# Optimization experiments

Measured on AMD Instinct MI355X. Metric: run time of the kernel, lower is better.

Reference implementation:

```python
import jax, jax.numpy as jnp
import numpy as np

N_NODES = 50000
N_EDGES = 600000
H_DIM = 128
N_RELS = 8
N_BASES = 4


def setup_inputs() -> dict:
    key = jax.random.key(0)
    ks = jax.random.split(key, 12)
    feats = jax.random.normal(ks[0], (N_NODES, H_DIM), dtype=jnp.float32)
    src = jax.random.randint(ks[1], (N_EDGES,), 0, N_NODES, dtype=jnp.int64)
    dst = jax.random.randint(ks[2], (N_EDGES,), 0, N_NODES, dtype=jnp.int64)
    etype = jax.random.randint(ks[3], (N_EDGES,), 0, N_RELS, dtype=jnp.int64)
    norm = jax.random.uniform(ks[4], (N_EDGES, 1), dtype=jnp.float32)
    s = 1.0 / np.sqrt(H_DIM)
    # layer 0 params (basis decomposition: W_r = sum_b comp[r,b] * basis[b])
    basis0 = jax.random.normal(ks[5], (N_BASES, H_DIM, H_DIM), dtype=jnp.float32) * s
    comp0 = jax.random.normal(ks[6], (N_RELS, N_BASES), dtype=jnp.float32)
    bias0 = jnp.zeros((H_DIM,), dtype=jnp.float32)
    # layer 1 params
    basis1 = jax.random.normal(ks[7], (N_BASES, H_DIM, H_DIM), dtype=jnp.float32) * s
    comp1 = jax.random.normal(ks[8], (N_RELS, N_BASES), dtype=jnp.float32)
    bias1 = jnp.zeros((H_DIM,), dtype=jnp.float32)
    return {"feats": feats, "src": src, "dst": dst, "etype": etype, "norm": norm,
            "basis0": basis0, "comp0": comp0, "bias0": bias0,
            "basis1": basis1, "comp1": comp1, "bias1": bias1}


def _rel_graph_conv(h, src, dst, etype, norm, basis, comp, bias):
    # basis-decomposed relation weights: [R, d_in, d_out]
    W = jnp.einsum('rb,bdo->rdo', comp, basis)
    # transform all nodes under every relation: [R, N, d_out]
    Hr = jnp.einsum('nd,rdo->rno', h, W)
    # gather per-edge message by (relation, source node), apply edge norm
    msg = Hr[etype, src] * norm  # [E, d_out]
    # scatter-sum into destination nodes
    agg = jax.ops.segment_sum(msg, dst, num_segments=h.shape[0])
    return jax.nn.relu(agg + bias)


def reference(feats, src, dst, etype, norm, basis0, comp0, bias0, basis1, comp1, bias1):
    h = _rel_graph_conv(feats, src, dst, etype, norm, basis0, comp0, bias0)
    h = _rel_graph_conv(h, src, dst, etype, norm, basis1, comp1, bias1)
    return h
```

## Files before the change

### kernel.cpp

```cpp
#include <hip/hip_runtime.h>

#define H    128
#define NB   4
#define DT   32

typedef __attribute__((ext_vector_type(8))) short short8;
typedef __attribute__((ext_vector_type(4))) float f32x4;

static __device__ __forceinline__ unsigned short f2bf(float f) {
    unsigned u = __float_as_uint(f);
    unsigned r = (u + 0x7fffu + ((u >> 16) & 1u)) >> 16;
    return (unsigned short)r;
}
static __device__ __forceinline__ float bf_lo(unsigned v) {
    return __uint_as_float((v & 0xffffu) << 16);
}
static __device__ __forceinline__ float bf_hi(unsigned v) {
    return __uint_as_float(v & 0xffff0000u);
}
static __device__ __forceinline__ float bfe(short s) {
    return __uint_as_float(((unsigned)(unsigned short)s) << 16);
}

__global__ __launch_bounds__(256) void zero_i(int* __restrict__ p, int n) {
    int i = blockIdx.x * 256 + threadIdx.x;
    if (i < n) p[i] = 0;
}

__global__ __launch_bounds__(256) void hist_rank(const int* __restrict__ dst,
                                                 int* __restrict__ counts,
                                                 int* __restrict__ rank, int E) {
    int e = blockIdx.x * 256 + threadIdx.x;
    if (e < E) rank[e] = atomicAdd(&counts[dst[e]], 1);
}

__global__ __launch_bounds__(1024) void scan_blocks(const int* __restrict__ counts,
                                                    int* __restrict__ partial,
                                                    int* __restrict__ blocksums, int n) {
    __shared__ int buf[1024];
    int tid = threadIdx.x;
    int i = blockIdx.x * 1024 + tid;
    buf[tid] = (i < n) ? counts[i] : 0;
    __syncthreads();
#pragma unroll
    for (int off = 1; off < 1024; off <<= 1) {
        int t = (tid >= off) ? buf[tid - off] : 0;
        __syncthreads();
        buf[tid] += t;
        __syncthreads();
    }
    if (i < n) partial[i] = buf[tid];
    if (tid == 1023) blocksums[blockIdx.x] = buf[1023];
}

__global__ __launch_bounds__(64) void scan_carry(int* __restrict__ blocksums, int nb) {
    int tid = threadIdx.x;
    int v = (tid < nb) ? blocksums[tid] : 0;
#pragma unroll
    for (int off = 1; off < 64; off <<= 1) {
        int t = __shfl_up(v, off);
        if (tid >= off) v += t;
    }
    if (tid < nb) blocksums[tid] = v;
}

__global__ __launch_bounds__(256) void scan_add(const int* __restrict__ partial,
                                                const int* __restrict__ blocksums,
                                                int* __restrict__ offs, int n) {
    int i = blockIdx.x * 256 + threadIdx.x;
    if (i >= n) return;
    int b = i >> 10;
    int carry = (b > 0) ? blocksums[b - 1] : 0;
    offs[i + 1] = partial[i] + carry;
    if (i == 0) offs[0] = 0;
}

__global__ __launch_bounds__(256) void scatter_edges(
        const int* __restrict__ src, const int* __restrict__ dst,
        const int* __restrict__ etype, const float* __restrict__ norm,
        const float* __restrict__ comp0, const float* __restrict__ comp1,
        const int* __restrict__ offs, const int* __restrict__ rank,
        uint4* __restrict__ er0, uint4* __restrict__ er1, int E) {
    int e = blockIdx.x * 256 + threadIdx.x;
    if (e >= E) return;
    int pos = offs[dst[e]] + rank[e];
    float w = norm[e];
    int et = etype[e];
    float4 c0 = *(const float4*)(comp0 + et * NB);
    float4 c1 = *(const float4*)(comp1 + et * NB);
    uint4 r0, r1;
    r0.x = (unsigned)src[e];
    r0.y = (unsigned)f2bf(w * c0.x) | ((unsigned)f2bf(w * c0.y) << 16);
    r0.z = (unsigned)f2bf(w * c0.z) | ((unsigned)f2bf(w * c0.w) << 16);
    r0.w = 0;
    r1.x = (unsigned)src[e];
    r1.y = (unsigned)f2bf(w * c1.x) | ((unsigned)f2bf(w * c1.y) << 16);
    r1.z = (unsigned)f2bf(w * c1.z) | ((unsigned)f2bf(w * c1.w) << 16);
    r1.w = 0;
    er0[pos] = r0;
    er1[pos] = r1;
}

__global__ __launch_bounds__(256) void convert_bf16(const float* __restrict__ in,
                                                    unsigned short* __restrict__ out, int n4) {
    int i = blockIdx.x * 256 + threadIdx.x;
    if (i >= n4) return;
    float4 v = ((const float4*)in)[i];
    ushort4 o;
    o.x = f2bf(v.x); o.y = f2bf(v.y); o.z = f2bf(v.z); o.w = f2bf(v.w);
    ((ushort4*)out)[i] = o;
}

__global__ __launch_bounds__(128) void make_wb(
        const float* __restrict__ basis0, const float* __restrict__ basis1,
        unsigned short* __restrict__ Wb) {
    int b = blockIdx.x;
    int d = blockIdx.y;
    int l = blockIdx.z;
    int o = threadIdx.x;
    const float* basis = l ? basis1 : basis0;
    float s = basis[((size_t)b * H + d) * H + o];
    Wb[((size_t)l * H + o) * (NB * H) + b * H + d] = f2bf(s);
}

#define EDGE_ACC(REC, HV) {                                             \
    float wa = bf_lo(REC.y), wb = bf_hi(REC.y);                         \
    float wc = bf_lo(REC.z), wd = bf_hi(REC.z);                         \
    _Pragma("unroll")                                                   \
    for (int c = 0; c < 8; ++c) {                                       \
        float f = bfe(HV[c]);                                           \
        a0[c] = fmaf(wa, f, a0[c]); a1[c] = fmaf(wb, f, a1[c]);         \
        a2[c] = fmaf(wc, f, a2[c]); a3[c] = fmaf(wd, f, a3[c]);         \
    } }

__global__ __launch_bounds__(512) void fused_layer(
        const unsigned short* __restrict__ hin,
        const int* __restrict__ offs,
        const uint4* __restrict__ er,
        const unsigned short* __restrict__ Wb,
        const float* __restrict__ bias,
        void* __restrict__ outp, int M, int write_bf16) {
    __shared__ char lds[DT * 1024];
    const int tid  = threadIdx.x;
    const int nl   = tid >> 4;
    const int ch   = tid & 15;
    const int v0   = blockIdx.x * DT;
    const int v    = v0 + nl;

    float a0[8], a1[8], a2[8], a3[8];
#pragma unroll
    for (int c = 0; c < 8; ++c) { a0[c] = 0.f; a1[c] = 0.f; a2[c] = 0.f; a3[c] = 0.f; }

    if (v < M) {
        const int beg = offs[v], end = offs[v + 1];
        int e = beg;
        for (; e + 2 <= end; e += 2) {
            uint4 r0 = er[e];
            uint4 r1 = er[e + 1];
            short8 h0 = *(const short8*)(hin + (size_t)r0.x * H + ch * 8);
            short8 h1 = *(const short8*)(hin + (size_t)r1.x * H + ch * 8);
            EDGE_ACC(r0, h0)
            EDGE_ACC(r1, h1)
        }
        if (e < end) {
            uint4 r0 = er[e];
            short8 h0 = *(const short8*)(hin + (size_t)r0.x * H + ch * 8);
            EDGE_ACC(r0, h0)
        }
    }

    {
        char* row = lds + nl * 1024;
        const int swz = (nl & 7) << 4;
        uint4 pk;
#define PACK(A) pk.x = (unsigned)f2bf(A[0]) | ((unsigned)f2bf(A[1]) << 16); \
                pk.y = (unsigned)f2bf(A[2]) | ((unsigned)f2bf(A[3]) << 16); \
                pk.z = (unsigned)f2bf(A[4]) | ((unsigned)f2bf(A[5]) << 16); \
                pk.w = (unsigned)f2bf(A[6]) | ((unsigned)f2bf(A[7]) << 16);
        PACK(a0) *(uint4*)(row + ((0 * 256 + ch * 16) ^ swz)) = pk;
        PACK(a1) *(uint4*)(row + ((1 * 256 + ch * 16) ^ swz)) = pk;
        PACK(a2) *(uint4*)(row + ((2 * 256 + ch * 16) ^ swz)) = pk;
        PACK(a3) *(uint4*)(row + ((3 * 256 + ch * 16) ^ swz)) = pk;
#undef PACK
    }
    __syncthreads();

    const int wid  = tid >> 6;
    const int lane = tid & 63;
    const int n0 = wid * 16;
    const int lr = lane & 15;
    const int lg = lane >> 4;
    const char* bbase = (const char*)Wb + (size_t)(n0 + lr) * (NB * H) * 2;
    const int swz = (lr & 7) << 4;

    f32x4 acc0 = (f32x4){0.f, 0.f, 0.f, 0.f};
    f32x4 acc1 = (f32x4){0.f, 0.f, 0.f, 0.f};
#pragma unroll
    for (int ks = 0; ks < 16; ++ks) {
        const int kb = ks * 64 + lg * 16;
        short8 b  = *(const short8*)(bbase + kb);
        short8 av0 = *(const short8*)(lds + (lr)      * 1024 + (kb ^ swz));
        short8 av1 = *(const short8*)(lds + (16 + lr) * 1024 + (kb ^ swz));
        acc0 = __builtin_amdgcn_mfma_f32_16x16x32_bf16(av0, b, acc0, 0, 0, 0);
        acc1 = __builtin_amdgcn_mfma_f32_16x16x32_bf16(av1, b, acc1, 0, 0, 0);
    }

    const float bcol = bias[n0 + lr];
#pragma unroll
    for (int m = 0; m < 2; ++m) {
        const f32x4 a = m ? acc1 : acc0;
#pragma unroll
        for (int j = 0; j < 4; ++j) {
            const int rl   = m * 16 + lg * 4 + j;
            const int grow = v0 + rl;
            if (grow < M) {
                float val = fmaxf(a[j] + bcol, 0.f);
                if (write_bf16)
                    ((unsigned short*)outp)[(size_t)grow * H + n0 + lr] = f2bf(val);
                else
                    ((float*)outp)[(size_t)grow * H + n0 + lr] = val;
            }
        }
    }
}

extern "C" void kernel_launch(void* const* d_in, const int* in_sizes, int n_in,
                              void* d_out, int out_size, void* d_ws, size_t ws_size,
                              hipStream_t stream) {
    const float* feats  = (const float*)d_in[0];
    const int*   src    = (const int*)  d_in[1];
    const int*   dst    = (const int*)  d_in[2];
    const int*   etype  = (const int*)  d_in[3];
    const float* norm   = (const float*)d_in[4];
    const float* basis0 = (const float*)d_in[5];
    const float* comp0  = (const float*)d_in[6];
    const float* bias0  = (const float*)d_in[7];
    const float* basis1 = (const float*)d_in[8];
    const float* comp1  = (const float*)d_in[9];
    const float* bias1  = (const float*)d_in[10];
    float* out = (float*)d_out;

    const int M = in_sizes[0] / H;
    const int E = in_sizes[1];

    char* ws = (char*)d_ws;
    size_t cur = 0;
    auto take = [&](size_t bytes) { void* p = ws + cur; cur += (bytes + 255) & ~(size_t)255; return p; };
    unsigned short* hbf  = (unsigned short*)take((size_t)M * H * 2);
    unsigned short* h1bf = (unsigned short*)take((size_t)M * H * 2);
    unsigned short* Wb   = (unsigned short*)take((size_t)2 * H * NB * H * 2);
    int*   counts  = (int*)take((size_t)M * 4);
    int*   offs    = (int*)take((size_t)(M + 1) * 4);
    int*   partial = (int*)take((size_t)M * 4);
    int*   bsums   = (int*)take((size_t)64 * 4);
    int*   rank    = (int*)take((size_t)E * 4);
    uint4* er0     = (uint4*)take((size_t)E * 16);
    uint4* er1     = (uint4*)take((size_t)E * 16);

    dim3 blk(256);
    int mb  = (M + 255) / 256;
    int eb  = (E + 255) / 256;
    int n4  = M * H / 4;
    int cb  = (n4 + 255) / 256;
    int nsb = (M + 1023) / 1024;
    int fb  = (M + DT - 1) / DT;

    zero_i       <<<mb, blk, 0, stream>>>(counts, M);
    hist_rank    <<<eb, blk, 0, stream>>>(dst, counts, rank, E);
    scan_blocks  <<<nsb, 1024, 0, stream>>>(counts, partial, bsums, M);
    scan_carry   <<<1, 64, 0, stream>>>(bsums, nsb);
    scan_add     <<<mb, blk, 0, stream>>>(partial, bsums, offs, M);
    scatter_edges<<<eb, blk, 0, stream>>>(src, dst, etype, norm, comp0, comp1,
                                          offs, rank, er0, er1, E);
    convert_bf16 <<<cb, blk, 0, stream>>>(feats, hbf, n4);
    make_wb      <<<dim3(NB, H, 2), 128, 0, stream>>>(basis0, basis1, Wb);

    fused_layer<<<fb, 512, 0, stream>>>(hbf, offs, er0, Wb, bias0, h1bf, M, 1);
    fused_layer<<<fb, 512, 0, stream>>>(h1bf, offs, er1,
                                        Wb + (size_t)H * NB * H, bias1, out, M, 0);
}
```

Baseline: 191.6 us.

## Split each node's edge list across two thread groups and halve node tile

Each block now handles 16 nodes instead of 32, with two 16-thread groups per node taking alternating edges. The two partial bf16 sums are added in LDS before a single 16-row MFMA pass. This doubles the grid size and shortens each thread's serial gather chain, aiming to hide gather latency and balance degree skew better. The cost is half the MFMA work per block plus an extra LDS reduction and barrier, and an additional bf16 rounding of the partial sums. The zeroing kernel is also replaced with hipMemsetAsync.

```diff
diff --git a/kernel.cpp b/kernel.cpp
--- a/kernel.cpp
+++ b/kernel.cpp
@@ -2,7 +2,7 @@
 
 #define H    128
 #define NB   4
-#define DT   32
+#define DT   16
 
 typedef __attribute__((ext_vector_type(8))) short short8;
 typedef __attribute__((ext_vector_type(4))) float f32x4;
@@ -21,10 +21,10 @@
 static __device__ __forceinline__ float bfe(short s) {
     return __uint_as_float(((unsigned)(unsigned short)s) << 16);
 }
-
-__global__ __launch_bounds__(256) void zero_i(int* __restrict__ p, int n) {
-    int i = blockIdx.x * 256 + threadIdx.x;
-    if (i < n) p[i] = 0;
+static __device__ __forceinline__ unsigned bfadd2(unsigned a, unsigned b) {
+    float lo = bf_lo(a) + bf_lo(b);
+    float hi = bf_hi(a) + bf_hi(b);
+    return (unsigned)f2bf(lo) | ((unsigned)f2bf(hi) << 16);
 }
 
 __global__ __launch_bounds__(256) void hist_rank(const int* __restrict__ dst,
@@ -123,7 +123,7 @@
     Wb[((size_t)l * H + o) * (NB * H) + b * H + d] = f2bf(s);
 }
 
-#define EDGE_ACC(REC, HV) {                                             \
+#define EACC(REC, HV) {                                                 \
     float wa = bf_lo(REC.y), wb = bf_hi(REC.y);                         \
     float wc = bf_lo(REC.z), wd = bf_hi(REC.z);                         \
     _Pragma("unroll")                                                   \
@@ -140,12 +140,14 @@
         const unsigned short* __restrict__ Wb,
         const float* __restrict__ bias,
         void* __restrict__ outp, int M, int write_bf16) {
-    __shared__ char lds[DT * 1024];
+    __shared__ char lds[32 * 1024];
     const int tid  = threadIdx.x;
-    const int nl   = tid >> 4;
+    const int slot = tid >> 4;
     const int ch   = tid & 15;
+    const int n    = slot & 15;
+    const int hh   = slot >> 4;
     const int v0   = blockIdx.x * DT;
-    const int v    = v0 + nl;
+    const int v    = v0 + n;
 
     float a0[8], a1[8], a2[8], a3[8];
 #pragma unroll
@@ -153,25 +155,25 @@
 
     if (v < M) {
         const int beg = offs[v], end = offs[v + 1];
-        int e = beg;
-        for (; e + 2 <= end; e += 2) {
+        int e = beg + hh;
+        for (; e + 2 < end; e += 4) {
             uint4 r0 = er[e];
-            uint4 r1 = er[e + 1];
+            uint4 r1 = er[e + 2];
             short8 h0 = *(const short8*)(hin + (size_t)r0.x * H + ch * 8);
             short8 h1 = *(const short8*)(hin + (size_t)r1.x * H + ch * 8);
-            EDGE_ACC(r0, h0)
-            EDGE_ACC(r1, h1)
+            EACC(r0, h0)
+            EACC(r1, h1)
         }
         if (e < end) {
             uint4 r0 = er[e];
             short8 h0 = *(const short8*)(hin + (size_t)r0.x * H + ch * 8);
-            EDGE_ACC(r0, h0)
+            EACC(r0, h0)
         }
     }
 
     {
-        char* row = lds + nl * 1024;
-        const int swz = (nl & 7) << 4;
+        char* row = lds + slot * 1024;
+        const int swz = (slot & 7) << 4;
         uint4 pk;
 #define PACK(A) pk.x = (unsigned)f2bf(A[0]) | ((unsigned)f2bf(A[1]) << 16); \
                 pk.y = (unsigned)f2bf(A[2]) | ((unsigned)f2bf(A[3]) << 16); \
@@ -185,41 +187,52 @@
     }
     __syncthreads();
 
+    {
+        const int mn = tid >> 5;
+        const int mc = tid & 31;
+        char*       p0 = lds + mn * 1024 + mc * 32;
+        const char* p1 = lds + (16 + mn) * 1024 + mc * 32;
+        uint4 x0 = *(uint4*)p0;
+        uint4 x1 = *(const uint4*)p1;
+        uint4 y0 = *(uint4*)(p0 + 16);
+        uint4 y1 = *(const uint4*)(p1 + 16);
+        x0.x = bfadd2(x0.x, x1.x); x0.y = bfadd2(x0.y, x1.y);
+        x0.z = bfadd2(x0.z, x1.z); x0.w = bfadd2(x0.w, x1.w);
+        y0.x = bfadd2(y0.x, y1.x); y0.y = bfadd2(y0.y, y1.y);
+        y0.z = bfadd2(y0.z, y1.z); y0.w = bfadd2(y0.w, y1.w);
+        *(uint4*)p0 = x0;
+        *(uint4*)(p0 + 16) = y0;
+    }
+    __syncthreads();
+
     const int wid  = tid >> 6;
     const int lane = tid & 63;
-    const int n0 = wid * 16;
     const int lr = lane & 15;
     const int lg = lane >> 4;
+    const int n0 = wid * 16;
     const char* bbase = (const char*)Wb + (size_t)(n0 + lr) * (NB * H) * 2;
+    const char* abase = lds + lr * 1024;
     const int swz = (lr & 7) << 4;
 
-    f32x4 acc0 = (f32x4){0.f, 0.f, 0.f, 0.f};
-    f32x4 acc1 = (f32x4){0.f, 0.f, 0.f, 0.f};
+    f32x4 acc = (f32x4){0.f, 0.f, 0.f, 0.f};
 #pragma unroll
     for (int ks = 0; ks < 16; ++ks) {
         const int kb = ks * 64 + lg * 16;
-        short8 b  = *(const short8*)(bbase + kb);
-        short8 av0 = *(const short8*)(lds + (lr)      * 1024 + (kb ^ swz));
-        short8 av1 = *(const short8*)(lds + (16 + lr) * 1024 + (kb ^ swz));
-        acc0 = __builtin_amdgcn_mfma_f32_16x16x32_bf16(av0, b, acc0, 0, 0, 0);
-        acc1 = __builtin_amdgcn_mfma_f32_16x16x32_bf16(av1, b, acc1, 0, 0, 0);
-    }
-
-    const float bcol = bias[n0 + lr];
-#pragma unroll
-    for (int m = 0; m < 2; ++m) {
-        const f32x4 a = m ? acc1 : acc0;
-#pragma unroll
-        for (int j = 0; j < 4; ++j) {
-            const int rl   = m * 16 + lg * 4 + j;
-            const int grow = v0 + rl;
-            if (grow < M) {
-                float val = fmaxf(a[j] + bcol, 0.f);
-                if (write_bf16)
-                    ((unsigned short*)outp)[(size_t)grow * H + n0 + lr] = f2bf(val);
-                else
-                    ((float*)outp)[(size_t)grow * H + n0 + lr] = val;
-            }
+        short8 a = *(const short8*)(abase + (kb ^ swz));
+        short8 b = *(const short8*)(bbase + kb);
+        acc = __builtin_amdgcn_mfma_f32_16x16x32_bf16(a, b, acc, 0, 0, 0);
+    }
+
+    const float bc = bias[n0 + lr];
+#pragma unroll
+    for (int j = 0; j < 4; ++j) {
+        const int grow = v0 + lg * 4 + j;
+        if (grow < M) {
+            float val = fmaxf(acc[j] + bc, 0.f);
+            if (write_bf16)
+                ((unsigned short*)outp)[(size_t)grow * H + n0 + lr] = f2bf(val);
+            else
+                ((float*)outp)[(size_t)grow * H + n0 + lr] = val;
         }
     }
 }
@@ -258,14 +271,14 @@
     uint4* er1     = (uint4*)take((size_t)E * 16);
 
     dim3 blk(256);
-    int mb  = (M + 255) / 256;
     int eb  = (E + 255) / 256;
     int n4  = M * H / 4;
     int cb  = (n4 + 255) / 256;
+    int mb  = (M + 255) / 256;
     int nsb = (M + 1023) / 1024;
     int fb  = (M + DT - 1) / DT;
 
-    zero_i       <<<mb, blk, 0, stream>>>(counts, M);
+    hipMemsetAsync(counts, 0, (size_t)M * 4, stream);
     hist_rank    <<<eb, blk, 0, stream>>>(dst, counts, rank, E);
     scan_blocks  <<<nsb, 1024, 0, stream>>>(counts, partial, bsums, M);
     scan_carry   <<<1, 64, 0, stream>>>(bsums, nsb);
```

After: 232.3 us. +21.3%, slower.
